# Optimization experiments

Measured on AMD Instinct MI355X. Metric: run time of the kernel, lower is better.

Reference implementation:

```python
import jax, jax.numpy as jnp
import numpy as np

B, N, F, T = 16, 1024, 32, 12
K, FC, FT, TS, D = 3, 64, 64, 1, 16
THETA_THR = 0.6
LN_EPS = 1e-5


def setup_inputs() -> dict:
    key = jax.random.key(0)
    ks = jax.random.split(key, 20)
    r = lambda i, shape, s=0.1: jax.random.normal(ks[i], shape, dtype=jnp.float32) * s
    return dict(
        x=jax.random.normal(ks[0], (B, N, F, T), dtype=jnp.float32),
        node_embeddings=r(1, (N, D), 1.0),
        W1=r(2, (T,)), W2=r(3, (F, T)), W3=r(4, (F,)),
        bs=r(5, (1, N, N)), Vs=r(6, (N, N)),
        U1=r(7, (N,)), U2=r(8, (F, N)), U3=r(9, (F,)),
        be=r(10, (1, T, T)), Ve=r(11, (T, T)),
        Theta=r(12, (K, F, FC)),
        tc_v=r(13, (FT, FC, 1, 3)), tc_g=jnp.ones((FT,), jnp.float32), tc_b=r(14, (FT,)),
        rc_w=r(15, (FT, F, 1, 1)), rc_b=r(16, (FT,)),
        ln_w=jnp.ones((FT,), jnp.float32), ln_b=jnp.zeros((FT,), jnp.float32),
    )


def _forward(x, node_embeddings, W1, W2, W3, bs, Vs, U1, U2, U3, be, Ve,
             Theta, tc_v, tc_g, tc_b, rc_w, rc_b, ln_w, ln_b):
    b, n, f, t = x.shape
    k_order = Theta.shape[0]

    # --- temporal attention: E (B,T,T) ---
    lhs = jnp.einsum('bnft,n->btf', x, U1) @ U2                # (B,T,N)
    rhs = jnp.einsum('f,bnft->bnt', U3, x)                     # (B,N,T)
    prod = jnp.einsum('btn,bnu->btu', lhs, rhs)                # (B,T,T)
    E = jnp.einsum('ts,bsu->btu', Ve, jax.nn.sigmoid(prod + be))
    E = jax.nn.softmax(E, axis=1)

    # x_TAt = reshape(B, N*F, T) @ E  (equivalent einsum over t)
    x_TAt = jnp.einsum('bnft,btu->bnfu', x, E)                 # (B,N,F,T)

    # --- sparse spatial attention on x_TAt: (B,N,N) ---
    l2 = jnp.einsum('bnft,t->bnf', x_TAt, W1) @ W2             # (B,N,T)
    r2 = jnp.einsum('f,bnft->btn', W3, x_TAt)                  # (B,T,N)
    prod2 = jnp.einsum('bnt,btm->bnm', l2, r2)                 # (B,N,N)
    S = jnp.einsum('nm,bmk->bnk', Vs, jax.nn.sigmoid(prod2 + bs))
    Sn = jax.nn.softmax(S, axis=1)
    thr = jnp.mean(Sn) / THETA_THR
    spat = jnp.where(Sn < thr, jnp.zeros_like(Sn), Sn)         # Sparse_S_normalized

    # --- K-order adaptive graph conv with attention mask ---
    sup = jax.nn.softmax(jax.nn.relu(node_embeddings @ node_embeddings.T), axis=1)
    polys = [jnp.eye(n, dtype=x.dtype), sup]
    for k in range(2, k_order):
        polys.append(2.0 * sup @ polys[-1] - polys[-2])
    out = jnp.zeros((b, t, n, Theta.shape[2]), x.dtype)
    for k in range(k_order):
        A = polys[k][None] * spat                              # (B,N,N)
        h = jnp.einsum('bnm,bnft->btmf', A, x)                 # A^T @ x per timestep
        out = out + jnp.einsum('btmf,fo->btmo', h, Theta[k])
    gcn = jax.nn.relu(out)                                     # (B,T,N,FC)

    # --- time conv (weight-normed 1x3) + residual 1x1 conv ---
    vnorm = jnp.sqrt(jnp.sum(tc_v * tc_v, axis=(1, 2, 3), keepdims=True))
    w = tc_g[:, None, None, None] * tc_v / vnorm
    inp = gcn.transpose(0, 3, 2, 1)                            # (B,FC,N,T)
    tco = jax.lax.conv_general_dilated(
        inp, w, (1, TS), ((0, 0), (1, 1)),
        dimension_numbers=('NCHW', 'OIHW', 'NCHW')) + tc_b[None, :, None, None]
    res = jax.lax.conv_general_dilated(
        x.transpose(0, 2, 1, 3), rc_w, (1, TS), ((0, 0), (0, 0)),
        dimension_numbers=('NCHW', 'OIHW', 'NCHW')) + rc_b[None, :, None, None]

    # --- layernorm over channel dim ---
    y = (res + tco).transpose(0, 3, 2, 1)                      # (B,T,N,FT)
    mu = jnp.mean(y, axis=-1, keepdims=True)
    var = jnp.var(y, axis=-1, keepdims=True)
    y = (y - mu) / jnp.sqrt(var + LN_EPS) * ln_w + ln_b
    x_res = y.transpose(0, 2, 3, 1)                            # (B,N,FT,T)
    return x_res, spat


def reference(x, node_embeddings, W1, W2, W3, bs, Vs, U1, U2, U3, be, Ve,
              Theta, tc_v, tc_g, tc_b, rc_w, rc_b, ln_w, ln_b):
    return _forward(x, node_embeddings, W1, W2, W3, bs, Vs, U1, U2, U3, be, Ve,
                    Theta, tc_v, tc_g, tc_b, rc_w, rc_b, ln_w, ln_b)
```

## Files before the change

kernel.cpp:

```cpp
#include <hip/hip_runtime.h>
#include <math.h>

#define NB 16
#define NN 1024
#define NF 32
#define NT 12
#define NFC 64
#define NFT 64

typedef __attribute__((ext_vector_type(8))) short bf16x8;
typedef __attribute__((ext_vector_type(4))) float f32x4;

__device__ inline unsigned short cvt_bf(float f) {
    unsigned int u = __float_as_uint(f);
    u += 0x7fff + ((u >> 16) & 1);
    return (unsigned short)(u >> 16);
}
__device__ inline float bf2f(unsigned short u) {
    return __uint_as_float(((unsigned int)u) << 16);
}
__device__ inline void gll16(const short* g, short* l) {
    __builtin_amdgcn_global_load_lds((const __attribute__((address_space(1))) void*)g,
                                     (__attribute__((address_space(3))) void*)l, 16, 0, 0);
}

__global__ __launch_bounds__(384) void k_pre(const float* __restrict__ x,
                                             const float* __restrict__ U1,
                                             const float* __restrict__ U3,
                                             const float* __restrict__ W3,
                                             float* __restrict__ lhs_pre,
                                             float* __restrict__ rhs,
                                             float* __restrict__ rr3,
                                             unsigned short* __restrict__ Xrow)
{
    __shared__ float xs[8 * 384];
    int b = blockIdx.x, ch = blockIdx.y, tid = threadIdx.x;
    float acc = 0.f;
    for (int c8 = 0; c8 < 8; c8++) {
        int n0 = ch * 64 + c8 * 8;
        size_t r0 = (size_t)b * NN + n0;
        __syncthreads();
        for (int i = 0; i < 8; i++) xs[i * 384 + tid] = x[(r0 + i) * 384 + tid];
        __syncthreads();
        for (int i = 0; i < 8; i++) acc += xs[i * 384 + tid] * U1[n0 + i];
        for (int idx = tid; idx < 1536; idx += 384) {
            int row = idx / 192, jj = (idx - row * 192) * 2;
            unsigned int w = (unsigned int)cvt_bf(xs[row * 384 + jj])
                           | ((unsigned int)cvt_bf(xs[row * 384 + jj + 1]) << 16);
            *(unsigned int*)(Xrow + (r0 + row) * 384 + jj) = w;
        }
        if (tid < 192) {
            int half = tid / 96;
            int r = tid - half * 96;
            int i = r / 12, t = r - i * 12;
            const float* wv = half ? W3 : U3;
            float s = 0.f;
            for (int f = 0; f < 32; f++) s += wv[f] * xs[i * 384 + f * 12 + t];
            float* outp = half ? rr3 : rhs;
            outp[(r0 + i) * 12 + t] = s;
        }
    }
    int f = tid / 12, t = tid - f * 12;
    atomicAdd(&lhs_pre[b * 384 + t * 32 + f], acc);
}

__global__ __launch_bounds__(256) void k_lhs(const float* __restrict__ lhs_pre,
                                             const float* __restrict__ U2,
                                             float* __restrict__ lhs)
{
    int bt = blockIdx.x;
    int tid = threadIdx.x;
    __shared__ float lp[32];
    if (tid < 32) lp[tid] = lhs_pre[bt * 32 + tid];
    __syncthreads();
    for (int q = 0; q < 4; q++) {
        int n = q * 256 + tid;
        float a = 0.f;
        for (int f = 0; f < 32; f++) a += lp[f] * U2[f * NN + n];
        lhs[(size_t)bt * NN + n] = a;
    }
}

__global__ __launch_bounds__(64) void k_prod(const float* __restrict__ lhs,
                                             const float* __restrict__ rhs,
                                             float* __restrict__ prod)
{
    int blk = blockIdx.x;
    int b = blk / 144, r = blk - b * 144;
    int s = r / 12, u = r - s * 12;
    int tid = threadIdx.x;
    float p = 0.f;
    for (int n = tid; n < NN; n += 64)
        p += lhs[((size_t)b * 12 + s) * NN + n] * rhs[((size_t)b * NN + n) * 12 + u];
    for (int o = 32; o > 0; o >>= 1) p += __shfl_xor(p, o);
    if (tid == 0) prod[blk] = p;
}

__global__ __launch_bounds__(192) void k_E(const float* __restrict__ prod,
                                           const float* __restrict__ be,
                                           const float* __restrict__ Ve,
                                           const float* __restrict__ W1,
                                           float* __restrict__ E,
                                           float* __restrict__ EW1)
{
    int b = blockIdx.x, tid = threadIdx.x;
    __shared__ float ssig[144], sE[144], mx[12], sm[12];
    if (tid < 144) ssig[tid] = 1.f / (1.f + expf(-(prod[b * 144 + tid] + be[tid])));
    __syncthreads();
    if (tid < 144) {
        int t = tid / 12, u = tid - t * 12;
        float a = 0.f;
        for (int s2 = 0; s2 < 12; s2++) a += Ve[t * 12 + s2] * ssig[s2 * 12 + u];
        sE[tid] = a;
    }
    __syncthreads();
    if (tid < 12) {
        float m = -1e30f;
        for (int t = 0; t < 12; t++) m = fmaxf(m, sE[t * 12 + tid]);
        float s = 0.f;
        for (int t = 0; t < 12; t++) s += expf(sE[t * 12 + tid] - m);
        mx[tid] = m; sm[tid] = s;
    }
    __syncthreads();
    float val = 0.f;
    if (tid < 144) {
        int u = tid % 12;
        val = expf(sE[tid] - mx[u]) / sm[u];
        E[b * 144 + tid] = val;
    }
    __syncthreads();
    if (tid < 144) sE[tid] = val;
    __syncthreads();
    if (tid < 12) {
        float a = 0.f;
        for (int u = 0; u < 12; u++) a += sE[tid * 12 + u] * W1[u];
        EW1[b * 12 + tid] = a;
    }
}

__global__ __launch_bounds__(384) void k_l2r2x(const unsigned short* __restrict__ Xrow,
                                               const float* __restrict__ rr3,
                                               const float* __restrict__ E,
                                               const float* __restrict__ EW1,
                                               const float* __restrict__ W2,
                                               float* __restrict__ l2,
                                               float* __restrict__ r2)
{
    __shared__ float xs[8 * 384];
    __shared__ float Es[144], ew[12], rrs[96], lp[8][32];
    int b = blockIdx.y, tid = threadIdx.x;
    int n0 = blockIdx.x * 8;
    size_t r0 = (size_t)b * NN + n0;
    if (tid < 144) Es[tid] = E[b * 144 + tid];
    if (tid < 12) ew[tid] = EW1[b * 12 + tid];
    if (tid < 96) rrs[tid] = rr3[(r0 + tid / 12) * 12 + (tid % 12)];
    const unsigned int* Xr = (const unsigned int*)(Xrow + r0 * 384);
    for (int i2 = tid; i2 < 1536; i2 += 384) {
        unsigned int w = Xr[i2];
        xs[2 * i2]     = bf2f((unsigned short)(w & 0xffff));
        xs[2 * i2 + 1] = bf2f((unsigned short)(w >> 16));
    }
    __syncthreads();
    if (tid < 256) {
        int i = tid >> 5, f = tid & 31;
        float a = 0.f;
#pragma unroll
        for (int t = 0; t < 12; t++) a += xs[i * 384 + f * 12 + t] * ew[t];
        lp[i][f] = a;
    }
    __syncthreads();
    if (tid < 96) {
        int i = tid / 12, u = tid - i * 12;
        float a = 0.f;
        for (int f = 0; f < 32; f++) a += lp[i][f] * W2[f * 12 + u];
        l2[(r0 + i) * 12 + u] = a;
        float rv = 0.f;
#pragma unroll
        for (int t = 0; t < 12; t++) rv += rrs[i * 12 + t] * Es[t * 12 + u];
        r2[((size_t)b * 12 + u) * NN + n0 + i] = rv;
    }
}

__global__ __launch_bounds__(256) void k_xt(const unsigned short* __restrict__ Xrow,
                                            unsigned short* __restrict__ Xt)
{
    __shared__ unsigned short tl[64][66];
    int b = blockIdx.z;
    int n0 = blockIdx.y * 64, j0 = blockIdx.x * 64;
    int tid = threadIdx.x;
    int c = tid & 63, r0 = tid >> 6;
    for (int i = 0; i < 16; i++) {
        int r = r0 + i * 4;
        tl[r][c] = Xrow[((size_t)b * NN + n0 + r) * 384 + j0 + c];
    }
    __syncthreads();
    int c2 = tid & 31, r4 = tid >> 5;
    unsigned short* ob = Xt + ((size_t)b * 384 + j0) * NN + n0;
    for (int i = 0; i < 8; i++) {
        int jr = r4 + i * 8;
        unsigned int v0 = (unsigned int)tl[2 * c2][jr] | ((unsigned int)tl[2 * c2 + 1][jr] << 16);
        *(unsigned int*)(ob + (size_t)jr * NN + 2 * c2) = v0;
    }
}

__global__ __launch_bounds__(256) void k_Ptile(const float* __restrict__ l2,
                                               const float* __restrict__ r2,
                                               const float* __restrict__ bsin,
                                               unsigned short* __restrict__ Pt)
{
    __shared__ float l2s[64][13];
    __shared__ float r2s[12][64];
    __shared__ float bsS[64][65];
    int k0 = blockIdx.x * 64, m0 = blockIdx.y * 64, b = blockIdx.z;
    int tid = threadIdx.x;
    for (int i = tid; i < 768; i += 256) {
        int r = i / 12, t = i - r * 12;
        l2s[r][t] = l2[((size_t)b * NN + m0 + r) * 12 + t];
    }
    for (int i = tid; i < 768; i += 256) {
        int t = i >> 6, k = i & 63;
        r2s[t][k] = r2[((size_t)b * 12 + t) * NN + k0 + k];
    }
    for (int i = tid; i < 4096; i += 256) {
        int r = i >> 6, c = i & 63;
        bsS[r][c] = bsin[(size_t)(m0 + r) * NN + k0 + c];
    }
    __syncthreads();
    int m = tid & 63, kg = tid >> 6;
    float lv[12];
#pragma unroll
    for (int t = 0; t < 12; t++) lv[t] = l2s[m][t];
#pragma unroll
    for (int s = 0; s < 16; s++) {
        int kl = kg * 16 + s;
        float p = bsS[m][kl];
#pragma unroll
        for (int t = 0; t < 12; t++) p += lv[t] * r2s[t][kl];
        float sg = 1.f / (1.f + expf(-p));
        Pt[((size_t)b * NN + k0 + kl) * NN + m0 + m] = cvt_bf(sg);
    }
}

__global__ __launch_bounds__(256) void k_cvt(const float* __restrict__ s,
                                             unsigned short* __restrict__ d)
{
    size_t i = ((size_t)blockIdx.x * 256 + threadIdx.x) * 4;
    float4 v = *(const float4*)(s + i);
    unsigned int p0 = (unsigned int)cvt_bf(v.x) | ((unsigned int)cvt_bf(v.y) << 16);
    unsigned int p1 = (unsigned int)cvt_bf(v.z) | ((unsigned int)cvt_bf(v.w) << 16);
    *(unsigned int*)(d + i) = p0;
    *(unsigned int*)(d + i + 2) = p1;
}

__global__ __launch_bounds__(256) void k_tb16(const unsigned short* __restrict__ s,
                                              unsigned short* __restrict__ d)
{
    __shared__ unsigned short tl[64][65];
    int r0 = blockIdx.y * 64, c0 = blockIdx.x * 64;
    int tid = threadIdx.x;
    int c = tid & 63, rr = tid >> 6;
    for (int i = 0; i < 16; i++)
        tl[rr + i * 4][c] = s[(size_t)(r0 + rr + i * 4) * NN + c0 + c];
    __syncthreads();
    for (int i = 0; i < 16; i++)
        d[(size_t)(c0 + rr + i * 4) * NN + r0 + c] = tl[c][rr + i * 4];
}

template<int MODE>
__global__ __launch_bounds__(256) void mgemm(const short* __restrict__ A,
                                             const short* __restrict__ B,
                                             void* __restrict__ Cv,
                                             int Kd, int kchunk,
                                             int ldA, int ldB, int ldC,
                                             long sA, long sB, long sC,
                                             float* __restrict__ colsum)
{
    int bz = blockIdx.z;
    const short* Ab = A + (size_t)bz * sA;
    const short* Bb = B + (size_t)bz * sB;
    int i0 = blockIdx.y * 128, j0 = blockIdx.x * 128;
    __shared__ short sm[16384];
    int tid = threadIdx.x;
    int ln = tid & 63, wv = tid >> 6;
    int wm = (wv >> 1) * 64, wn = (wv & 1) * 64;
    int fr = ln & 15, fk = ln >> 4;
    f32x4 acc[4][4];
#pragma unroll
    for (int a = 0; a < 4; a++)
#pragma unroll
        for (int b2 = 0; b2 < 4; b2++) acc[a][b2] = (f32x4)(0.f);

    int k_lo = 0, k_hi = Kd;
    if constexpr (MODE == 3) { k_lo = bz * kchunk; k_hi = k_lo + kchunk; }

    for (int k0 = k_lo; k0 < k_hi; k0 += 64) {
#pragma unroll
        for (int q = 0; q < 4; q++) {
            int e = q * 2048 + tid * 8;
            const short* src = Ab + (size_t)(i0 + (e >> 6)) * ldA + k0 + (e & 63);
            gll16(src, sm + e);
        }
#pragma unroll
        for (int q = 0; q < 4; q++) {
            int e = q * 2048 + tid * 8;
            const short* src = Bb + (size_t)(j0 + (e >> 6)) * ldB + k0 + (e & 63);
            gll16(src, sm + 8192 + e);
        }
        __syncthreads();
#pragma unroll
        for (int ks = 0; ks < 2; ks++) {
            bf16x8 av[4], bv[4];
#pragma unroll
            for (int mi = 0; mi < 4; mi++)
                av[mi] = *(const bf16x8*)(sm + (wm + mi * 16 + fr) * 64 + ks * 32 + fk * 8);
#pragma unroll
            for (int nj = 0; nj < 4; nj++)
                bv[nj] = *(const bf16x8*)(sm + 8192 + (wn + nj * 16 + fr) * 64 + ks * 32 + fk * 8);
#pragma unroll
            for (int mi = 0; mi < 4; mi++)
#pragma unroll
                for (int nj = 0; nj < 4; nj++)
                    acc[mi][nj] = __builtin_amdgcn_mfma_f32_16x16x32_bf16(av[mi], bv[nj], acc[mi][nj], 0, 0, 0);
        }
        __syncthreads();
    }
    if constexpr (MODE == 2) {
        float* Cb = (float*)Cv + (size_t)bz * sC;
#pragma unroll
        for (int nj = 0; nj < 4; nj++) {
            float cs = 0.f;
            int col = j0 + wn + nj * 16 + fr;
#pragma unroll
            for (int mi = 0; mi < 4; mi++) {
                int row = i0 + wm + mi * 16 + fk * 4;
#pragma unroll
                for (int r = 0; r < 4; r++) {
                    float e = expf(acc[mi][nj][r]);
                    Cb[(size_t)(row + r) * ldC + col] = e;
                    cs += e;
                }
            }
            cs += __shfl_xor(cs, 16);
            cs += __shfl_xor(cs, 32);
            if (ln < 16) atomicAdd(&colsum[(size_t)bz * NN + col], cs);
        }
    } else if constexpr (MODE == 3) {
        float* Cb = (float*)Cv;
#pragma unroll
        for (int mi = 0; mi < 4; mi++)
#pragma unroll
            for (int nj = 0; nj < 4; nj++) {
                int row = i0 + wm + mi * 16 + fk * 4;
                int col = j0 + wn + nj * 16 + fr;
#pragma unroll
                for (int r = 0; r < 4; r++)
                    atomicAdd(&Cb[(size_t)(row + r) * ldC + col], acc[mi][nj][r]);
            }
    }
}

__global__ __launch_bounds__(256) void mgemm_h(const short* __restrict__ A,
                                               const short* __restrict__ B,
                                               unsigned short* __restrict__ C)
{
    int id = blockIdx.x;
    int xcd = id & 7, jj = id >> 3;
    int b = (xcd << 1) | (jj / 24);
    int r = jj % 24;
    int i0 = (r / 3) * 128, j0 = (r % 3) * 128;
    const short* Ab = A + (size_t)b * NN * NN;
    const short* Bb = B + (size_t)b * 384 * NN;
    __shared__ short sm[16384];
    int tid = threadIdx.x;
    int ln = tid & 63, wv = tid >> 6;
    int wm = (wv >> 1) * 64, wn = (wv & 1) * 64;
    int fr = ln & 15, fk = ln >> 4;
    f32x4 acc[4][4];
#pragma unroll
    for (int a = 0; a < 4; a++)
#pragma unroll
        for (int b2 = 0; b2 < 4; b2++) acc[a][b2] = (f32x4)(0.f);

    for (int k0 = 0; k0 < NN; k0 += 64) {
#pragma unroll
        for (int q = 0; q < 4; q++) {
            int e = q * 2048 + tid * 8;
            gll16(Ab + (size_t)(i0 + (e >> 6)) * NN + k0 + (e & 63), sm + e);
        }
#pragma unroll
        for (int q = 0; q < 4; q++) {
            int e = q * 2048 + tid * 8;
            gll16(Bb + (size_t)(j0 + (e >> 6)) * NN + k0 + (e & 63), sm + 8192 + e);
        }
        __syncthreads();
#pragma unroll
        for (int ks = 0; ks < 2; ks++) {
            bf16x8 av[4], bv[4];
#pragma unroll
            for (int mi = 0; mi < 4; mi++)
                av[mi] = *(const bf16x8*)(sm + (wm + mi * 16 + fr) * 64 + ks * 32 + fk * 8);
#pragma unroll
            for (int nj = 0; nj < 4; nj++)
                bv[nj] = *(const bf16x8*)(sm + 8192 + (wn + nj * 16 + fr) * 64 + ks * 32 + fk * 8);
#pragma unroll
            for (int mi = 0; mi < 4; mi++)
#pragma unroll
                for (int nj = 0; nj < 4; nj++)
                    acc[mi][nj] = __builtin_amdgcn_mfma_f32_16x16x32_bf16(av[mi], bv[nj], acc[mi][nj], 0, 0, 0);
        }
        __syncthreads();
    }
#pragma unroll
    for (int mi = 0; mi < 4; mi++)
#pragma unroll
        for (int nj = 0; nj < 4; nj++) {
            int row = i0 + wm + mi * 16 + fk * 4;
            int col = j0 + wn + nj * 16 + fr;
#pragma unroll
            for (int r2 = 0; r2 < 4; r2++)
                C[((size_t)b * NN + row + r2) * 384 + col] = cvt_bf(acc[mi][nj][r2]);
        }
}

__global__ __launch_bounds__(256) void k_normprep2(float* __restrict__ spat,
                                                   const float* __restrict__ colsum,
                                                   const float* __restrict__ sup,
                                                   const float* __restrict__ supsq,
                                                   unsigned short* __restrict__ At1,
                                                   unsigned short* __restrict__ At2,
                                                   float* __restrict__ sdiag)
{
    __shared__ unsigned short t1[64][66];
    __shared__ unsigned short t2[64][66];
    int b = blockIdx.z;
    int n0 = blockIdx.y * 64, m0 = blockIdx.x * 64;
    int tid = threadIdx.x;
    int c = tid & 63, r0 = tid >> 6;
    const float thr = (1.0f / 1024.0f) / 0.6f;
    float inv = 1.f / colsum[(size_t)b * NN + m0 + c];
    float* sp = spat + (size_t)b * NN * NN;
    for (int i = 0; i < 16; i++) {
        int r = r0 + i * 4;
        size_t idx = (size_t)(n0 + r) * NN + m0 + c;
        float v = sp[idx] * inv;
        v = (v < thr) ? 0.f : v;
        sp[idx] = v;
        if (n0 + r == m0 + c) sdiag[(size_t)b * NN + n0 + r] = v;
        t1[r][c] = cvt_bf(sup[(size_t)(n0 + r) * NN + m0 + c] * v);
        float p2 = 2.f * supsq[(size_t)(n0 + r) * NN + m0 + c]
                 - (((n0 + r) == (m0 + c)) ? 1.f : 0.f);
        t2[r][c] = cvt_bf(p2 * v);
    }
    __syncthreads();
    int c2 = tid & 31, r4 = tid >> 5;
    size_t ob = ((size_t)b * NN + m0) * NN + n0;
    for (int i = 0; i < 8; i++) {
        int rr = r4 + i * 8;
        unsigned int v1 = (unsigned int)t1[2 * c2][rr] | ((unsigned int)t1[2 * c2 + 1][rr] << 16);
        unsigned int v2 = (unsigned int)t2[2 * c2][rr] | ((unsigned int)t2[2 * c2 + 1][rr] << 16);
        *(unsigned int*)(At1 + ob + (size_t)rr * NN + 2 * c2) = v1;
        *(unsigned int*)(At2 + ob + (size_t)rr * NN + 2 * c2) = v2;
    }
}

__global__ __launch_bounds__(256) void k_sup(const float* __restrict__ emb,
                                             float* __restrict__ sup,
                                             unsigned short* __restrict__ supB)
{
    int n = blockIdx.x, tid = threadIdx.x;
    __shared__ float en[16];
    if (tid < 16) en[tid] = emb[n * 16 + tid];
    __syncthreads();
    float v[4];
#pragma unroll
    for (int q = 0; q < 4; q++) {
        int m = q * 256 + tid;
        float d = 0.f;
#pragma unroll
        for (int dd = 0; dd < 16; dd++) d += en[dd] * emb[m * 16 + dd];
        v[q] = fmaxf(d, 0.f);
    }
    float mx = fmaxf(fmaxf(v[0], v[1]), fmaxf(v[2], v[3]));
    for (int o = 32; o > 0; o >>= 1) mx = fmaxf(mx, __shfl_xor(mx, o));
    __shared__ float red[4];
    if ((tid & 63) == 0) red[tid >> 6] = mx;
    __syncthreads();
    mx = fmaxf(fmaxf(red[0], red[1]), fmaxf(red[2], red[3]));
    float e[4];
    float s = 0.f;
#pragma unroll
    for (int q = 0; q < 4; q++) { e[q] = expf(v[q] - mx); s += e[q]; }
    for (int o = 32; o > 0; o >>= 1) s += __shfl_xor(s, o);
    __shared__ float red2[4];
    if ((tid & 63) == 0) red2[tid >> 6] = s;
    __syncthreads();
    s = red2[0] + red2[1] + red2[2] + red2[3];
    float inv = 1.f / s;
#pragma unroll
    for (int q = 0; q < 4; q++) {
        float val = e[q] * inv;
        sup[(size_t)n * NN + q * 256 + tid] = val;
        supB[(size_t)n * NN + q * 256 + tid] = cvt_bf(val);
    }
}

__global__ __launch_bounds__(256) void k_wprep(const float* __restrict__ tcv,
                                               const float* __restrict__ tcg,
                                               const float* __restrict__ Theta,
                                               const float* __restrict__ rcw,
                                               unsigned short* __restrict__ Wr,
                                               unsigned short* __restrict__ Th,
                                               unsigned short* __restrict__ Rc)
{
    int tid = threadIdx.x;
    if (blockIdx.x < 64) {
        int o = blockIdx.x;
        float t = 0.f, p = 0.f;
        if (tid < 192) { t = tcv[o * 192 + tid]; p = t * t; }
        for (int off = 32; off > 0; off >>= 1) p += __shfl_xor(p, off);
        __shared__ float wsr[3];
        if (tid < 192 && (tid & 63) == 0) wsr[tid >> 6] = p;
        __syncthreads();
        if (tid < 192) {
            float sum = wsr[0] + wsr[1] + wsr[2];
            int c = tid / 3, dt = tid - c * 3;
            Wr[o * 192 + dt * 64 + c] = cvt_bf(t * (tcg[o] / sqrtf(sum)));
        }
    } else {
        for (int i = tid; i < 6144; i += 256) {
            int o = i / 96, rem = i - o * 96;
            int kind = rem >> 5, f = rem & 31;
            Th[i] = cvt_bf(Theta[kind * 2048 + f * 64 + o]);
        }
        for (int i = tid; i < 2048; i += 256) Rc[i] = cvt_bf(rcw[i]);
    }
}

__global__ __launch_bounds__(256) void k_tail(const float* __restrict__ x,
                                              const unsigned short* __restrict__ h1,
                                              const unsigned short* __restrict__ h2,
                                              const float* __restrict__ sdiag,
                                              const unsigned short* __restrict__ Th,
                                              const unsigned short* __restrict__ Wr,
                                              const unsigned short* __restrict__ Rc,
                                              const float* __restrict__ tcb,
                                              const float* __restrict__ rcb,
                                              const float* __restrict__ lnw,
                                              const float* __restrict__ lnb,
                                              float* __restrict__ out)
{
    int b = blockIdx.y;
    int node0 = blockIdx.x * 4;
    int tid = threadIdx.x;
    int ln = tid & 63, wv = tid >> 6;
    int fr = ln & 15, fk = ln >> 4;

    __shared__ union {
        struct { unsigned short xt[1920], h1t[1920], h2t[1920], gcn[4032]; } a;
        float Y[48 * 65];
    } u;
    __shared__ float sdp[48];
    __shared__ float lnwS[64], lnbS[64], tbS[64];
    __shared__ float muS[48], rsS[48];

    size_t rowb = ((size_t)b * NN + node0) * 384;
    {
        const float2* xp = (const float2*)(x + rowb);
        const unsigned int* h1p = (const unsigned int*)(h1 + rowb);
        const unsigned int* h2p = (const unsigned int*)(h2 + rowb);
        for (int q = tid; q < 768; q += 256) {
            int j0 = q * 2;
            int node = j0 / 384, j = j0 - node * 384;
            int f = j / 12, t = j - f * 12;
            int t2 = t + 1, f2 = f;
            if (t2 == 12) { t2 = 0; f2 = f + 1; }
            int la0 = node * 480 + t * 40 + f;
            int la1 = node * 480 + t2 * 40 + f2;
            float2 xv = xp[q];
            unsigned int w1 = h1p[q], w2 = h2p[q];
            u.a.xt[la0] = cvt_bf(xv.x);  u.a.xt[la1] = cvt_bf(xv.y);
            u.a.h1t[la0] = (unsigned short)(w1 & 0xffff); u.a.h1t[la1] = (unsigned short)(w1 >> 16);
            u.a.h2t[la0] = (unsigned short)(w2 & 0xffff); u.a.h2t[la1] = (unsigned short)(w2 >> 16);
        }
    }
    for (int i = tid; i < 576; i += 256) {
        int node = i / 144, r = i - node * 144;
        int rr = (r < 72) ? 0 : 13;
        u.a.gcn[node * 1008 + rr * 72 + (r % 72)] = 0;
    }
    if (tid < 48) sdp[tid] = sdiag[(size_t)b * NN + node0 + tid / 12];
    if (tid < 64) { lnwS[tid] = lnw[tid]; lnbS[tid] = lnb[tid]; tbS[tid] = tcb[tid] + rcb[tid]; }

    int ocol = wv * 16 + fr;
    bf16x8 bTh[3], bWr[6], bRc;
#pragma unroll
    for (int kb = 0; kb < 3; kb++)
        bTh[kb] = *(const bf16x8*)((const short*)Th + (size_t)ocol * 96 + kb * 32 + fk * 8);
#pragma unroll
    for (int kb = 0; kb < 6; kb++)
        bWr[kb] = *(const bf16x8*)((const short*)Wr + (size_t)ocol * 192 + kb * 32 + fk * 8);
    bRc = *(const bf16x8*)((const short*)Rc + (size_t)ocol * 32 + fk * 8);

    int na[3], ta[3];
#pragma unroll
    for (int rb = 0; rb < 3; rb++) {
        int p = rb * 16 + fr;
        na[rb] = p / 12; ta[rb] = p - na[rb] * 12;
    }
    __syncthreads();

    f32x4 acc[3];
#pragma unroll
    for (int rb = 0; rb < 3; rb++) {
        int ax = na[rb] * 480 + ta[rb] * 40 + fk * 8;
        bf16x8 avx = *(const bf16x8*)(u.a.xt + ax);
        f32x4 z = (f32x4)(0.f);
        acc[rb] = __builtin_amdgcn_mfma_f32_16x16x32_bf16(avx, bTh[0], z, 0, 0, 0);
#pragma unroll
        for (int r = 0; r < 4; r++) acc[rb][r] *= sdp[rb * 16 + fk * 4 + r];
        bf16x8 av1 = *(const bf16x8*)(u.a.h1t + ax);
        acc[rb] = __builtin_amdgcn_mfma_f32_16x16x32_bf16(av1, bTh[1], acc[rb], 0, 0, 0);
        bf16x8 av2 = *(const bf16x8*)(u.a.h2t + ax);
        acc[rb] = __builtin_amdgcn_mfma_f32_16x16x32_bf16(av2, bTh[2], acc[rb], 0, 0, 0);
    }
#pragma unroll
    for (int rb = 0; rb < 3; rb++) {
#pragma unroll
        for (int r = 0; r < 4; r++) {
            int pc = rb * 16 + fk * 4 + r;
            int nc = pc / 12, tc2 = pc - nc * 12;
            u.a.gcn[nc * 1008 + (tc2 + 1) * 72 + wv * 16 + fr] = cvt_bf(fmaxf(acc[rb][r], 0.f));
        }
    }
    __syncthreads();
#pragma unroll
    for (int rb = 0; rb < 3; rb++) {
        f32x4 a2 = (f32x4)(0.f);
#pragma unroll
        for (int kb = 0; kb < 6; kb++) {
            int dt = kb >> 1, c0 = (kb & 1) * 32;
            bf16x8 ag = *(const bf16x8*)(u.a.gcn + na[rb] * 1008 + (ta[rb] + dt) * 72 + c0 + fk * 8);
            a2 = __builtin_amdgcn_mfma_f32_16x16x32_bf16(ag, bWr[kb], a2, 0, 0, 0);
        }
        int ax = na[rb] * 480 + ta[rb] * 40 + fk * 8;
        bf16x8 avx = *(const bf16x8*)(u.a.xt + ax);
        acc[rb] = __builtin_amdgcn_mfma_f32_16x16x32_bf16(avx, bRc, a2, 0, 0, 0);
    }
    __syncthreads();
    float tb = tbS[ocol];
#pragma unroll
    for (int rb = 0; rb < 3; rb++)
#pragma unroll
        for (int r = 0; r < 4; r++)
            u.Y[(rb * 16 + fk * 4 + r) * 65 + ocol] = acc[rb][r] + tb;
    __syncthreads();
    if (tid < 48) {
        float s = 0.f, s2 = 0.f;
        for (int o = 0; o < 64; o++) {
            float v = u.Y[tid * 65 + o];
            s += v; s2 += v * v;
        }
        float mm = s * (1.f / 64.f);
        float var = s2 * (1.f / 64.f) - mm * mm;
        muS[tid] = mm; rsS[tid] = rsqrtf(var + 1e-5f);
    }
    __syncthreads();
    float2* obv = (float2*)(out + rowb * 2);
    for (int q = tid; q < 1536; q += 256) {
        int i = q * 2;
        int node = i / 768, rr = i - node * 768;
        int o = rr / 12, t = rr - o * 12;
        int p0 = node * 12 + t;
        float v0 = (u.Y[p0 * 65 + o] - muS[p0]) * rsS[p0] * lnwS[o] + lnbS[o];
        int t1 = t + 1, o1 = o;
        if (t1 == 12) { t1 = 0; o1 = o + 1; }
        int p1 = node * 12 + t1;
        float v1 = (u.Y[p1 * 65 + o1] - muS[p1]) * rsS[p1] * lnwS[o1] + lnbS[o1];
        float2 pk; pk.x = v0; pk.y = v1;
        obv[q] = pk;
    }
}

extern "C" void kernel_launch(void* const* d_in, const int* in_sizes, int n_in,
                              void* d_out, int out_size, void* d_ws, size_t ws_size,
                              hipStream_t stream)
{
    const float* x    = (const float*)d_in[0];
    const float* emb  = (const float*)d_in[1];
    const float* W1   = (const float*)d_in[2];
    const float* W2   = (const float*)d_in[3];
    const float* W3   = (const float*)d_in[4];
    const float* bs   = (const float*)d_in[5];
    const float* Vs   = (const float*)d_in[6];
    const float* U1   = (const float*)d_in[7];
    const float* U2   = (const float*)d_in[8];
    const float* U3   = (const float*)d_in[9];
    const float* be   = (const float*)d_in[10];
    const float* Ve   = (const float*)d_in[11];
    const float* Theta= (const float*)d_in[12];
    const float* tcv  = (const float*)d_in[13];
    const float* tcg  = (const float*)d_in[14];
    const float* tcb  = (const float*)d_in[15];
    const float* rcw  = (const float*)d_in[16];
    const float* rcb  = (const float*)d_in[17];
    const float* lnw  = (const float*)d_in[18];
    const float* lnb  = (const float*)d_in[19];

    float* xres = (float*)d_out;
    float* spat = xres + (size_t)NB * NN * NFT * NT;

    char* base = (char*)d_ws;
    unsigned short* Xrow = (unsigned short*)(base + 0);
    unsigned short* Pt   = (unsigned short*)(base + 0);
    unsigned short* supB = (unsigned short*)(base + 0);
    unsigned short* supT = (unsigned short*)(base + 2097152);
    unsigned short* At1  = (unsigned short*)(base + 0);
    unsigned short* At2  = (unsigned short*)xres;
    unsigned short* Xt  = (unsigned short*)(base + 33554432);
    unsigned short* h1  = (unsigned short*)(base + 46137344);
    unsigned short* h2  = (unsigned short*)(base + 58720256);
    unsigned short* Vsb = (unsigned short*)(base + 71303168);
    float* colsum  = (float*)(base + 73400320);
    float* sdiag   = (float*)(base + 73465856);
    float* sup     = (float*)(base + 77594624);
    float* supsq   = (float*)(base + 81788928);
    float* lhs_pre = (float*)(base + 85983232);
    float* lhs     = (float*)(base + 86007808);
    float* rhs     = (float*)(base + 86794240);
    float* rr3     = (float*)(base + 87580672);
    float* prod    = (float*)(base + 88367104);
    float* E       = (float*)(base + 88376320);
    float* EW1     = (float*)(base + 88385536);
    float* l2      = (float*)(base + 88386560);
    float* r2      = (float*)(base + 89172992);
    unsigned short* Wr = (unsigned short*)(base + 89959424);
    unsigned short* Th = (unsigned short*)(base + 89984000);
    unsigned short* Rc = (unsigned short*)(base + 89996288);

    hipMemsetAsync(lhs_pre, 0, 6144 * sizeof(float), stream);
    hipMemsetAsync(supsq, 0, (size_t)NN * NN * sizeof(float), stream);

    k_pre<<<dim3(16, 16), 384, 0, stream>>>(x, U1, U3, W3, lhs_pre, rhs, rr3, Xrow);
    k_lhs<<<192, 256, 0, stream>>>(lhs_pre, U2, lhs);
    k_prod<<<2304, 64, 0, stream>>>(lhs, rhs, prod);
    k_E<<<16, 192, 0, stream>>>(prod, be, Ve, W1, E, EW1);
    k_l2r2x<<<dim3(128, 16), 384, 0, stream>>>(Xrow, rr3, E, EW1, W2, l2, r2);
    k_xt<<<dim3(6, 16, 16), 256, 0, stream>>>(Xrow, Xt);
    k_Ptile<<<dim3(16, 16, 16), 256, 0, stream>>>(l2, r2, bs, Pt);
    k_cvt<<<1024, 256, 0, stream>>>(Vs, Vsb);
    hipMemsetAsync(colsum, 0, (size_t)NB * NN * sizeof(float), stream);
    mgemm<2><<<dim3(8, 8, 16), 256, 0, stream>>>((const short*)Vsb, (const short*)Pt,
        (void*)spat, NN, 0, NN, NN, NN, 0L, (long)NN * NN, (long)NN * NN, colsum);
    k_sup<<<1024, 256, 0, stream>>>(emb, sup, supB);
    k_tb16<<<dim3(16, 16), 256, 0, stream>>>(supB, supT);
    mgemm<3><<<dim3(8, 8, 4), 256, 0, stream>>>((const short*)supB, (const short*)supT,
        (void*)supsq, NN, 256, NN, NN, NN, 0L, 0L, 0L, nullptr);
    k_normprep2<<<dim3(16, 16, 16), 256, 0, stream>>>(spat, colsum, sup, supsq, At1, At2, sdiag);
    mgemm_h<<<384, 256, 0, stream>>>((const short*)At1, (const short*)Xt, h1);
    mgemm_h<<<384, 256, 0, stream>>>((const short*)At2, (const short*)Xt, h2);
    k_wprep<<<65, 256, 0, stream>>>(tcv, tcg, Theta, rcw, Wr, Th, Rc);
    k_tail<<<dim3(256, 16), 256, 0, stream>>>(x, h1, h2, sdiag, Th, Wr, Rc,
                                              tcb, rcb, lnw, lnb, xres);
}
```

Measured before the change: 336.9 us.

## Replace batched spatial-attention GEMM with 256x256-tile double-buffered swizzled MFMA kernel

Adds a dedicated 512-thread GEMM for the Vs x sigmoid(P) batched product. It uses 256x256 output tiles, a double-buffered LDS pipeline fed by global_load_lds, XOR-swizzled LDS layout to avoid bank conflicts, fine-grained phase interleaving of loads with MFMAs, and s_setprio. The exp and column-sum epilogue is unchanged. The aim is more data reuse per tile and hiding global latency behind compute, at the cost of 128KB LDS per block, only 256 blocks, and heavy register pressure.

```diff
diff --git a/kernel.cpp b/kernel.cpp
--- a/kernel.cpp
+++ b/kernel.cpp
@@ -266,6 +266,135 @@
         d[(size_t)(c0 + rr + i * 4) * NN + r0 + c] = tl[c][rr + i * 4];
 }
 
+__device__ inline void stage2(const short* __restrict__ g, int grow0, int gk0,
+                              short* dstbase, int tid)
+{
+#pragma unroll
+    for (int o = 0; o < 2; o++) {
+        int y = o * 8192 + tid * 16;
+        int rowh = y >> 7;
+        int colb = (y & 127) ^ ((rowh & 7) << 4);
+        const short* src = g + (size_t)(grow0 + rowh) * NN + gk0 + (colb >> 1);
+        gll16(src, dstbase + (y >> 1));
+    }
+}
+
+__global__ __launch_bounds__(512, 2) void sgemm8(const short* __restrict__ A,
+                                                 const short* __restrict__ Bm,
+                                                 float* __restrict__ C,
+                                                 float* __restrict__ colsum)
+{
+    int bz = blockIdx.z;
+    const short* Bb = Bm + (size_t)bz * NN * NN;
+    int i0 = blockIdx.y * 256, j0 = blockIdx.x * 256;
+    __shared__ short sm[65536];
+    int tid = threadIdx.x;
+    int ln = tid & 63, wv = tid >> 6;
+    int wm = (wv >> 2) * 128, wn = (wv & 3) * 64;
+    int fr = ln & 15, fk = ln >> 4;
+    int ahalf = wv >> 2;
+    int bhalf = wn >> 7;
+    int bcol = wn & 64;
+    int swz = (fr & 7) << 4;
+    int kcol0 = ((fk * 16) ^ swz) >> 1;
+    int kcol1 = ((64 + fk * 16) ^ swz) >> 1;
+
+    f32x4 acc[8][4];
+#pragma unroll
+    for (int m = 0; m < 8; m++)
+#pragma unroll
+        for (int n = 0; n < 4; n++) acc[m][n] = (f32x4)(0.f);
+
+    stage2(Bb, j0 + 0,   0,  sm + 16384,        tid);
+    stage2(Bb, j0 + 128, 0,  sm + 16384 + 8192, tid);
+    stage2(A,  i0 + 0,   0,  sm + 0,            tid);
+    stage2(A,  i0 + 128, 0,  sm + 8192,         tid);
+    stage2(Bb, j0 + 0,   64, sm + 32768 + 16384,        tid);
+    stage2(Bb, j0 + 128, 64, sm + 32768 + 16384 + 8192, tid);
+    asm volatile("s_waitcnt vmcnt(4)" ::: "memory");
+    __builtin_amdgcn_s_barrier();
+
+    for (int i = 0; i < 8; i++) {
+        bf16x8 bv[8];
+#pragma unroll
+        for (int ph = 0; ph < 8; ph++) {
+            int t = 2 * i + (ph >> 2);
+            int p = t & 1;
+            int q = ph & 3;
+            int abase = p * 32768 + ahalf * 8192;
+            int bbase = p * 32768 + 16384 + bhalf * 8192;
+            if (q == 0) {
+#pragma unroll
+                for (int nj = 0; nj < 4; nj++) {
+                    int browh = bcol + nj * 16 + fr;
+                    bv[nj * 2 + 0] = *(const bf16x8*)(sm + bbase + browh * 64 + kcol0);
+                    bv[nj * 2 + 1] = *(const bf16x8*)(sm + bbase + browh * 64 + kcol1);
+                }
+            }
+            bf16x8 av[4];
+#pragma unroll
+            for (int m2 = 0; m2 < 2; m2++) {
+                int rowh = (2 * q + m2) * 16 + fr;
+                av[m2 * 2 + 0] = *(const bf16x8*)(sm + abase + rowh * 64 + kcol0);
+                av[m2 * 2 + 1] = *(const bf16x8*)(sm + abase + rowh * 64 + kcol1);
+            }
+            {
+                int st, smat, shalf;
+                if (ph == 0)      { st = 2 * i + 1; smat = 0; shalf = 0; }
+                else if (ph == 1) { st = 2 * i + 1; smat = 0; shalf = 1; }
+                else if (ph == 2) { st = 2 * i + 2; smat = 1; shalf = 0; }
+                else if (ph == 3) { st = 2 * i + 2; smat = 1; shalf = 1; }
+                else if (ph == 4) { st = 2 * i + 2; smat = 0; shalf = 0; }
+                else if (ph == 5) { st = 2 * i + 2; smat = 0; shalf = 1; }
+                else if (ph == 6) { st = 2 * i + 3; smat = 1; shalf = 0; }
+                else              { st = 2 * i + 3; smat = 1; shalf = 1; }
+                if (st < 16) {
+                    short* dst = sm + (st & 1) * 32768 + smat * 16384 + shalf * 8192;
+                    const short* g = smat ? Bb : A;
+                    int grow0 = (smat ? j0 : i0) + shalf * 128;
+                    stage2(g, grow0, st * 64, dst, tid);
+                }
+            }
+            __builtin_amdgcn_s_barrier();
+            __builtin_amdgcn_s_setprio(1);
+#pragma unroll
+            for (int m2 = 0; m2 < 2; m2++)
+#pragma unroll
+                for (int nj = 0; nj < 4; nj++) {
+                    acc[2 * q + m2][nj] = __builtin_amdgcn_mfma_f32_16x16x32_bf16(
+                        av[m2 * 2 + 0], bv[nj * 2 + 0], acc[2 * q + m2][nj], 0, 0, 0);
+                    acc[2 * q + m2][nj] = __builtin_amdgcn_mfma_f32_16x16x32_bf16(
+                        av[m2 * 2 + 1], bv[nj * 2 + 1], acc[2 * q + m2][nj], 0, 0, 0);
+                }
+            __builtin_amdgcn_s_setprio(0);
+            if (ph == 3 || ph == 7) {
+                if (i < 7) asm volatile("s_waitcnt vmcnt(4)" ::: "memory");
+                else       asm volatile("s_waitcnt vmcnt(0)" ::: "memory");
+            }
+            __builtin_amdgcn_s_barrier();
+        }
+    }
+    float* Cb = C + (size_t)bz * NN * NN;
+#pragma unroll
+    for (int nj = 0; nj < 4; nj++) {
+        int col = j0 + wn + nj * 16 + fr;
+        float cs = 0.f;
+#pragma unroll
+        for (int m = 0; m < 8; m++) {
+            int row = i0 + wm + m * 16 + fk * 4;
+#pragma unroll
+            for (int r = 0; r < 4; r++) {
+                float e = expf(acc[m][nj][r]);
+                Cb[(size_t)(row + r) * NN + col] = e;
+                cs += e;
+            }
+        }
+        cs += __shfl_xor(cs, 16);
+        cs += __shfl_xor(cs, 32);
+        if (ln < 16) atomicAdd(&colsum[(size_t)bz * NN + col], cs);
+    }
+}
+
 template<int MODE>
 __global__ __launch_bounds__(256) void mgemm(const short* __restrict__ A,
                                              const short* __restrict__ B,
@@ -324,27 +453,7 @@
         }
         __syncthreads();
     }
-    if constexpr (MODE == 2) {
-        float* Cb = (float*)Cv + (size_t)bz * sC;
-#pragma unroll
-        for (int nj = 0; nj < 4; nj++) {
-            float cs = 0.f;
-            int col = j0 + wn + nj * 16 + fr;
-#pragma unroll
-            for (int mi = 0; mi < 4; mi++) {
-                int row = i0 + wm + mi * 16 + fk * 4;
-#pragma unroll
-                for (int r = 0; r < 4; r++) {
-                    float e = expf(acc[mi][nj][r]);
-                    Cb[(size_t)(row + r) * ldC + col] = e;
-                    cs += e;
-                }
-            }
-            cs += __shfl_xor(cs, 16);
-            cs += __shfl_xor(cs, 32);
-            if (ln < 16) atomicAdd(&colsum[(size_t)bz * NN + col], cs);
-        }
-    } else if constexpr (MODE == 3) {
+    if constexpr (MODE == 3) {
         float* Cb = (float*)Cv;
 #pragma unroll
         for (int mi = 0; mi < 4; mi++)
@@ -749,8 +858,8 @@
     k_Ptile<<<dim3(16, 16, 16), 256, 0, stream>>>(l2, r2, bs, Pt);
     k_cvt<<<1024, 256, 0, stream>>>(Vs, Vsb);
     hipMemsetAsync(colsum, 0, (size_t)NB * NN * sizeof(float), stream);
-    mgemm<2><<<dim3(8, 8, 16), 256, 0, stream>>>((const short*)Vsb, (const short*)Pt,
-        (void*)spat, NN, 0, NN, NN, NN, 0L, (long)NN * NN, (long)NN * NN, colsum);
+    sgemm8<<<dim3(4, 4, 16), 512, 0, stream>>>((const short*)Vsb, (const short*)Pt,
+                                               spat, colsum);
     k_sup<<<1024, 256, 0, stream>>>(emb, sup, supB);
     k_tb16<<<dim3(16, 16), 256, 0, stream>>>(supB, supT);
     mgemm<3><<<dim3(8, 8, 4), 256, 0, stream>>>((const short*)supB, (const short*)supT,
```

Result: faster. 316.3 us (-6.1%).
